# Kernel tuning notes

Measured on AMD Instinct MI355X. Metric: run time of the kernel, lower is better.

## Reference

```python
import jax, jax.numpy as jnp
import numpy as np

H = 512   # hidden_size
L = 20    # num_labels
B, S = 32, 256


def _uniform(key, shape, k):
    return jax.random.uniform(key, shape, minval=-k, maxval=k, dtype=jnp.float32)


def setup_inputs() -> dict:
    key = jax.random.key(0)
    ks = iter(jax.random.split(key, 40))
    k = 1.0 / np.sqrt(H)
    inp = {
        "inputs": jax.random.normal(next(ks), (B, S, H), dtype=jnp.float32),
        "labels": jax.random.randint(next(ks), (B, S), 0, L),
        "mask": jnp.ones((B, S), dtype=jnp.int32),
    }
    for layer, din in ((0, H), (1, 2 * H)):
        for d in ("f", "b"):
            inp[f"w_ih_l{layer}{d}"] = _uniform(next(ks), (4 * H, din), k)
            inp[f"w_hh_l{layer}{d}"] = _uniform(next(ks), (4 * H, H), k)
            inp[f"b_ih_l{layer}{d}"] = _uniform(next(ks), (4 * H,), k)
            inp[f"b_hh_l{layer}{d}"] = _uniform(next(ks), (4 * H,), k)
    kf = 1.0 / np.sqrt(2 * H)
    inp["fc_w"] = _uniform(next(ks), (L, 2 * H), kf)
    inp["fc_b"] = _uniform(next(ks), (L,), kf)
    inp["trans_m"] = jax.random.normal(next(ks), (L, L), dtype=jnp.float32) * 0.1
    inp["start_scores"] = jax.random.normal(next(ks), (L,), dtype=jnp.float32) * 0.1
    inp["end_scores"] = jax.random.normal(next(ks), (L,), dtype=jnp.float32) * 0.1
    return inp


def _lstm_dir(x, wih, whh, bih, bhh, reverse):
    # x: [S, B, Din] -> hs: [S, B, H] (outputs in original time order)
    _, b, _ = x.shape
    hh = whh.shape[1]
    xw = jnp.einsum('sbd,gd->sbg', x, wih) + bih + bhh  # precompute input projections

    def step(carry, xt):
        h, c = carry
        g = xt + h @ whh.T  # [B, 4H]
        i, f, gg, o = jnp.split(g, 4, axis=-1)  # pytorch gate order i,f,g,o
        c = jax.nn.sigmoid(f) * c + jax.nn.sigmoid(i) * jnp.tanh(gg)
        h = jax.nn.sigmoid(o) * jnp.tanh(c)
        return (h, c), h

    init = (jnp.zeros((b, hh), x.dtype), jnp.zeros((b, hh), x.dtype))
    _, hs = jax.lax.scan(step, init, xw, reverse=reverse)
    return hs


def _crf_loss(logits, tags, maskf, trans, start, end):
    # logits [S,B,L], tags [S,B], maskf [S,B] float. Returns per-sample NLL [B].
    s, b, n = logits.shape
    # --- normalizer (forward algorithm) ---
    alpha0 = logits[0] + start  # [B, n]

    def step(alpha, inp):
        emit, m = inp  # emit [B,n], m [B]
        tmp = alpha[:, :, None] + trans[None, :, :] + emit[:, None, :]  # [B, from, to]
        new = jax.nn.logsumexp(tmp, axis=1)
        alpha = jnp.where(m[:, None] > 0, new, alpha)
        return alpha, None

    alpha, _ = jax.lax.scan(step, alpha0, (logits[1:], maskf[1:]))
    norm = jax.nn.logsumexp(alpha + end, axis=1)  # [B]
    # --- gold path score ---
    emit = jnp.take_along_axis(logits, tags[:, :, None], axis=2)[:, :, 0] * maskf  # [S,B]
    trans_sc = trans[tags[:-1], tags[1:]] * maskf[1:]  # [S-1,B]
    last_idx = maskf.sum(0).astype(jnp.int32) - 1  # [B]
    last_tags = tags[last_idx, jnp.arange(b)]
    gold = emit.sum(0) + trans_sc.sum(0) + start[tags[0]] + end[last_tags]
    return norm - gold


def reference(inputs, labels, mask,
              w_ih_l0f, w_hh_l0f, b_ih_l0f, b_hh_l0f,
              w_ih_l0b, w_hh_l0b, b_ih_l0b, b_hh_l0b,
              w_ih_l1f, w_hh_l1f, b_ih_l1f, b_hh_l1f,
              w_ih_l1b, w_hh_l1b, b_ih_l1b, b_hh_l1b,
              fc_w, fc_b, trans_m, start_scores, end_scores):
    x = jnp.transpose(inputs, (1, 0, 2))  # [S,B,H]
    h0 = jnp.concatenate([
        _lstm_dir(x, w_ih_l0f, w_hh_l0f, b_ih_l0f, b_hh_l0f, False),
        _lstm_dir(x, w_ih_l0b, w_hh_l0b, b_ih_l0b, b_hh_l0b, True),
    ], axis=-1)  # [S,B,2H]
    h1 = jnp.concatenate([
        _lstm_dir(h0, w_ih_l1f, w_hh_l1f, b_ih_l1f, b_hh_l1f, False),
        _lstm_dir(h0, w_ih_l1b, w_hh_l1b, b_ih_l1b, b_hh_l1b, True),
    ], axis=-1)  # [S,B,2H]
    logits = h1 @ fc_w.T + fc_b  # [S,B,L]
    tags = labels.T  # [S,B]
    maskf = mask.T.astype(logits.dtype)
    loss = _crf_loss(logits, tags, maskf, trans_m, start_scores, end_scores)
    return loss.mean()
```

## Files before the change

### kernel.cpp

```cpp
#include <hip/hip_runtime.h>

#define Sx 256
#define Bx 32
#define Hx 512
#define Gx 2048
#define Lx 20
#define Rx 8192

typedef __attribute__((ext_vector_type(8))) short short8;
typedef __attribute__((ext_vector_type(4))) float f32x4;
typedef __attribute__((ext_vector_type(16))) float f32x16;

__device__ __forceinline__ unsigned short f2bf(float f) {
  union { float f; unsigned u; } v; v.f = f;
  unsigned u = v.u;
  return (unsigned short)((u + 0x7fffu + ((u >> 16) & 1u)) >> 16);
}
__device__ __forceinline__ float bf2f(unsigned short h) {
  union { unsigned u; float f; } v; v.u = ((unsigned)h) << 16;
  return v.f;
}
__device__ __forceinline__ float bfh(unsigned long long x, int r) {
  return bf2f((unsigned short)((x >> (16 * r)) & 0xffffull));
}

__device__ __forceinline__ float fsigm(float x) {
  return __builtin_amdgcn_rcpf(1.0f + __builtin_amdgcn_exp2f(-1.44269504f * x));
}
__device__ __forceinline__ float ftanh(float x) {
  return __builtin_fmaf(-2.0f,
      __builtin_amdgcn_rcpf(1.0f + __builtin_amdgcn_exp2f(2.88539008f * x)), 1.0f);
}
#define L2E 1.44269504088896f
#define LN2 0.69314718055995f

#define GLD16(gp, lp) __builtin_amdgcn_global_load_lds( \
    (const __attribute__((address_space(1))) void*)(gp), \
    (__attribute__((address_space(3))) void*)(lp), 16, 0, 0)


__global__ void k_pack_x(const float* __restrict__ x, unsigned short* __restrict__ xbf) {
  int tid = blockIdx.x * 256 + threadIdx.x;
  int h = tid & (Hx - 1);
  int r = tid >> 9;
  int b = r & 31;
  int t = r >> 5;
  xbf[tid] = f2bf(x[(b * Sx + t) * Hx + h]);
}

__global__ __launch_bounds__(256) void k_prep(
    const float* __restrict__ s0, const float* __restrict__ s1,
    const float* __restrict__ s2, const float* __restrict__ s3,
    const float* __restrict__ s4, const float* __restrict__ s5,
    const float* __restrict__ s6, const float* __restrict__ s7,
    unsigned short* __restrict__ d0, unsigned short* __restrict__ d1,
    unsigned short* __restrict__ d2, unsigned short* __restrict__ d3,
    unsigned short* __restrict__ d4, unsigned short* __restrict__ d5,
    unsigned short* __restrict__ d6, unsigned short* __restrict__ d7,
    const float* __restrict__ ba0, const float* __restrict__ bb0, float* __restrict__ bo0,
    const float* __restrict__ ba1, const float* __restrict__ bb1, float* __restrict__ bo1,
    const float* __restrict__ ba2, const float* __restrict__ bb2, float* __restrict__ bo2,
    const float* __restrict__ ba3, const float* __restrict__ bb3, float* __restrict__ bo3)
{
  const int blk = blockIdx.x;
  const int tid = threadIdx.x;
  if (blk < 5120) {
    const float* srcs[8] = { s0, s1, s2, s3, s4, s5, s6, s7 };
    unsigned short* dsts[8] = { d0, d1, d2, d3, d4, d5, d6, d7 };
    size_t e0 = ((size_t)blk * 256 + tid) * 8;
    int m = (int)(e0 >> 20);
    int seg; size_t base;
    if (m < 4)      { seg = m; base = (size_t)m << 20; }
    else if (m < 6) { seg = 4; base = (size_t)4 << 20; }
    else if (m < 8) { seg = 5; base = (size_t)6 << 20; }
    else if (m == 8){ seg = 6; base = (size_t)8 << 20; }
    else            { seg = 7; base = (size_t)9 << 20; }
    size_t off = e0 - base;
    f32x4 a = *(const f32x4*)(srcs[seg] + off);
    f32x4 b = *(const f32x4*)(srcs[seg] + off + 4);
    short8 o;
    o[0] = (short)f2bf(a[0]); o[1] = (short)f2bf(a[1]);
    o[2] = (short)f2bf(a[2]); o[3] = (short)f2bf(a[3]);
    o[4] = (short)f2bf(b[0]); o[5] = (short)f2bf(b[1]);
    o[6] = (short)f2bf(b[2]); o[7] = (short)f2bf(b[3]);
    *(short8*)(dsts[seg] + off) = o;
  } else {
    int j = blk - 5120;
    const float* bas[4] = { ba0, ba1, ba2, ba3 };
    const float* bbs[4] = { bb0, bb1, bb2, bb3 };
    float* bos[4] = { bo0, bo1, bo2, bo3 };
    int i0 = tid * 8;
    f32x4 x0 = *(const f32x4*)(bas[j] + i0);
    f32x4 x1 = *(const f32x4*)(bas[j] + i0 + 4);
    f32x4 y0 = *(const f32x4*)(bbs[j] + i0);
    f32x4 y1 = *(const f32x4*)(bbs[j] + i0 + 4);
    *(f32x4*)(bos[j] + i0) = x0 + y0;
    *(f32x4*)(bos[j] + i0 + 4) = x1 + y1;
  }
}

__global__ __launch_bounds__(256) void k_gemm(
    const unsigned short* __restrict__ A,
    const unsigned short* __restrict__ Bw,
    const float* __restrict__ bias,
    unsigned short* __restrict__ C,
    int M, int N, int K)
{
  const int bn = blockIdx.x, bm = blockIdx.y;
  const int tid = threadIdx.x;
  const int w = tid >> 6, lane = tid & 63;
  const int wr = w >> 1, wc = w & 1;
  const int lo = lane & 15, qd = lane >> 4;

  __shared__ unsigned short As[128 * 64];
  __shared__ unsigned short Bs[128 * 64];

  f32x4 acc[4][4] = {};

  const int cis = (lane & 7) ^ (lane >> 3);
  const int ktn = K >> 6;
  for (int kt = 0; kt < ktn; ++kt) {
    __syncthreads();
#pragma unroll
    for (int p = 0; p < 4; ++p) {
      int rowb = w * 8 + p * 32;
      int row = rowb + (lane >> 3);
      GLD16(&A[(size_t)(bm * 128 + row) * K + kt * 64 + cis * 8], &As[rowb * 64]);
      GLD16(&Bw[(size_t)(bn * 128 + row) * K + kt * 64 + cis * 8], &Bs[rowb * 64]);
    }
    __syncthreads();
#pragma unroll
    for (int kk = 0; kk < 2; ++kk) {
      short8 af[4], bfr[4];
#pragma unroll
      for (int mi = 0; mi < 4; ++mi)
        af[mi] = *(const short8*)&As[(wr * 64 + mi * 16 + lo) * 64
                                     + (((kk * 4 + qd) ^ (lo & 7)) * 8)];
#pragma unroll
      for (int ni = 0; ni < 4; ++ni)
        bfr[ni] = *(const short8*)&Bs[(wc * 64 + ni * 16 + lo) * 64
                                      + (((kk * 4 + qd) ^ (lo & 7)) * 8)];
#pragma unroll
      for (int mi = 0; mi < 4; ++mi)
#pragma unroll
        for (int ni = 0; ni < 4; ++ni)
          acc[mi][ni] = __builtin_amdgcn_mfma_f32_16x16x32_bf16(af[mi], bfr[ni], acc[mi][ni], 0, 0, 0);
    }
  }
#pragma unroll
  for (int mi = 0; mi < 4; ++mi) {
#pragma unroll
    for (int ni = 0; ni < 4; ++ni) {
      int n = bn * 128 + wc * 64 + ni * 16 + lo;
      float bv = bias[n];
      int wsb = (n >> 4) & 31, cg = n >> 9, jl = n & 15;
      size_t base = (size_t)wsb * (Rx * 64) + (size_t)cg * 16 + jl;
#pragma unroll
      for (int r = 0; r < 4; ++r) {
        int m = bm * 128 + wr * 64 + mi * 16 + qd * 4 + r;
        C[base + (size_t)m * 64] = f2bf(acc[mi][ni][r] + bv);
      }
    }
  }
}

__global__ __launch_bounds__(256, 1) void k_lstm(
    const unsigned short* __restrict__ xwF,
    const unsigned short* __restrict__ xwB,
    const unsigned short* __restrict__ whF,
    const unsigned short* __restrict__ whB,
    unsigned short* __restrict__ hT,
    unsigned int* __restrict__ flags,
    unsigned int* __restrict__ done,
    const unsigned short* __restrict__ gWf,
    const unsigned short* __restrict__ gWb,
    const float* __restrict__ gBf,
    const float* __restrict__ gBb,
    unsigned short* __restrict__ gCf,
    unsigned short* __restrict__ gCb,
    unsigned int* __restrict__ wq,
    int gw)
{
  const int wg = blockIdx.x;
  const int tid = threadIdx.x;

  __shared__ unsigned short Ws[64 * 512];
  __shared__ unsigned widx;

  if (wg >= 64) {
    asm volatile("s_setprio 0");
    if (gw) {
      const int w = tid >> 6, lane = tid & 63;
      const int wr = w >> 1, wc = w & 1;
      const int lo = lane & 15, qd = lane >> 4;
      const int cis = (lane & 7) ^ (lane >> 3);
      for (;;) {
        if (tid == 0) widx = atomicAdd(wq, 1u);
        __syncthreads();
        unsigned idx = widx;
        __syncthreads();
        if (idx >= 2048u) break;
        int r = (int)(idx >> 5), sub = (int)(idx & 31);
        int dir1 = sub >> 4, bn = sub & 15;
        int bm = (r & 1) ? (32 - ((r + 1) >> 1)) : (32 + (r >> 1));
        unsigned tF = (unsigned)(4 * bm + 4), tB = (unsigned)(256 - 4 * bm);
        if (tid < 64) {
          for (;;) {
            unsigned v = __hip_atomic_load(flags + (lane >> 5) * 1024 + (lane & 31) * 32,
                                           __ATOMIC_RELAXED, __HIP_MEMORY_SCOPE_AGENT);
            unsigned tgt = (lane < 32) ? tF : tB;
            if (__all((int)(v >= tgt))) break;
            if (__hip_atomic_load(done, __ATOMIC_RELAXED, __HIP_MEMORY_SCOPE_AGENT) >= 64u)
              break;
            float aa = 1.0f;
#pragma unroll 4
            for (int i = 0; i < 512; ++i) aa = __builtin_fmaf(aa, 1.0000001f, 1e-7f);
            asm volatile("" :: "v"(aa));
          }
        }
        __syncthreads();
        const unsigned short* Bw = dir1 ? gWb : gWf;
        const float* bias = dir1 ? gBb : gBf;
        unsigned short* Cq = dir1 ? gCb : gCf;
        f32x4 acc[4][4] = {};
        for (int kt = 0; kt < 16; ++kt) {
          __syncthreads();
#pragma unroll
          for (int p = 0; p < 4; ++p) {
            int rowb = w * 8 + p * 32;
            int row = rowb + (lane >> 3);
            int grow = bm * 128 + row;
            int t2 = grow >> 5, b2 = grow & 31;
            int k = kt * 64 + cis * 8;
            int dirx = k >> 9, kk2 = k & 511;
            GLD16(&hT[(size_t)dirx * (Sx * 16384) + (size_t)t2 * 16384
                      + (size_t)(kk2 >> 3) * 256 + b2 * 8], &Ws[rowb * 64]);
            GLD16(&Bw[(size_t)(bn * 128 + row) * 1024 + kt * 64 + cis * 8],
                  &Ws[8192 + rowb * 64]);
          }
          __syncthreads();
#pragma unroll
          for (int kk = 0; kk < 2; ++kk) {
            short8 af[4], bfr[4];
#pragma unroll
            for (int mi = 0; mi < 4; ++mi)
              af[mi] = *(const short8*)&Ws[(wr * 64 + mi * 16 + lo) * 64
                                           + (((kk * 4 + qd) ^ (lo & 7)) * 8)];
#pragma unroll
            for (int ni = 0; ni < 4; ++ni)
              bfr[ni] = *(const short8*)&Ws[8192 + (wc * 64 + ni * 16 + lo) * 64
                                            + (((kk * 4 + qd) ^ (lo & 7)) * 8)];
#pragma unroll
            for (int mi = 0; mi < 4; ++mi)
#pragma unroll
              for (int ni = 0; ni < 4; ++ni)
                acc[mi][ni] = __builtin_amdgcn_mfma_f32_16x16x32_bf16(af[mi], bfr[ni], acc[mi][ni], 0, 0, 0);
          }
        }
#pragma unroll
        for (int mi = 0; mi < 4; ++mi) {
#pragma unroll
          for (int ni = 0; ni < 4; ++ni) {
            int n = bn * 128 + wc * 64 + ni * 16 + lo;
            float bv = bias[n];
            int wsb = (n >> 4) & 31, cg = n >> 9, jl = n & 15;
            size_t base = (size_t)wsb * (Rx * 64) + (size_t)cg * 16 + jl;
#pragma unroll
            for (int r2 = 0; r2 < 4; ++r2) {
              int m2 = bm * 128 + wr * 64 + mi * 16 + qd * 4 + r2;
              Cq[base + (size_t)m2 * 64] = f2bf(acc[mi][ni][r2] + bv);
            }
          }
        }
        __syncthreads();
      }
    }
    {
      float a = 1.0f + (float)tid, bm2 = 1.0000001f, cm = 1.0e-7f;
      for (;;) {
#pragma unroll 8
        for (int i = 0; i < 512; ++i) a = __builtin_fmaf(a, bm2, cm);
        if (__hip_atomic_load(done, __ATOMIC_RELAXED, __HIP_MEMORY_SCOPE_AGENT) >= 64u) break;
      }
      if (a == 123.456789f) ((volatile float*)hT)[0] = a;
    }
    return;
  }

  asm volatile("s_setprio 3");
  const int dir = wg >> 5;
  const int vs = wg & 31;
  const int j0 = vs * 16;
  const unsigned short* xw = (dir ? xwB : xwF) + (size_t)vs * (Rx * 64);
  const unsigned short* wh = dir ? whB : whF;
  unsigned short* hTd = hT + (size_t)dir * (Sx * 16384);
  unsigned int* fl = flags + dir * 32 * 32;

  {
    const int l6 = tid & 63;
#pragma unroll
    for (int i = 0; i < 16; ++i) {
      int rr = (tid >> 6) * 16 + i;
      int g = ((rr >> 4) << 9) + j0 + (rr & 15);
      int pc = l6 ^ (rr & 7);
      *(short8*)&Ws[rr * 512 + pc * 8] = *(const short8*)&wh[(size_t)g * Hx + l6 * 8];
    }
  }
  __syncthreads();
  if (tid >= 64) return;

  const int lane = tid;
  const int bn = lane & 31;
  const int q  = lane >> 5;

  float cst[2][4] = {};

  for (int s = 0; s < Sx; ++s) {
    const int t = dir ? (Sx - 1 - s) : s;

    const unsigned short* xwt = xw + ((size_t)t * 32 + bn) * 64 + q * 4;
    unsigned long long xg[4][2];
#pragma unroll
    for (int c = 0; c < 4; ++c)
#pragma unroll
      for (int jg = 0; jg < 2; ++jg)
        xg[c][jg] = *(const unsigned long long*)(xwt + c * 16 + jg * 8);
    __asm__ __volatile__("" ::: "memory");

    f32x16 acc0, acc1;

    if (s > 0) {
      const unsigned tgt = (unsigned)s;
      const int tp = dir ? (t + 1) : (t - 1);
      const unsigned short* hb = hTd + (size_t)tp * 16384 + lane * 8;

      short8 hreg[32];
      for (;;) {
        unsigned v = __hip_atomic_load(fl + (lane & 31) * 32,
                                       __ATOMIC_RELAXED, __HIP_MEMORY_SCOPE_AGENT);
#pragma unroll
        for (int ks = 0; ks < 32; ++ks)
          hreg[ks] = *(const short8*)(hb + ks * 512);
#pragma unroll
        for (int ks = 0; ks < 32; ++ks)
          asm volatile("" :: "v"(hreg[ks]));
        if (__all((int)(v >= tgt))) break;
        __asm__ __volatile__("" ::: "memory");
      }
      __builtin_amdgcn_sched_barrier(0);

      f32x16 a0 = {}, a1 = {}, b0 = {}, b1 = {};
#pragma unroll
      for (int ks = 0; ks < 32; ks += 2) {
        int lc0 = ks * 2 + q, lc1 = (ks + 1) * 2 + q;
        int pc0 = lc0 ^ (bn & 7), pc1 = lc1 ^ (bn & 7);
        short8 af00 = *(const short8*)&Ws[bn * 512 + pc0 * 8];
        short8 af10 = *(const short8*)&Ws[(32 + bn) * 512 + pc0 * 8];
        short8 af01 = *(const short8*)&Ws[bn * 512 + pc1 * 8];
        short8 af11 = *(const short8*)&Ws[(32 + bn) * 512 + pc1 * 8];
        a0 = __builtin_amdgcn_mfma_f32_32x32x16_bf16(af00, hreg[ks],     a0, 0, 0, 0);
        a1 = __builtin_amdgcn_mfma_f32_32x32x16_bf16(af10, hreg[ks],     a1, 0, 0, 0);
        b0 = __builtin_amdgcn_mfma_f32_32x32x16_bf16(af01, hreg[ks + 1], b0, 0, 0, 0);
        b1 = __builtin_amdgcn_mfma_f32_32x32x16_bf16(af11, hreg[ks + 1], b1, 0, 0, 0);
      }
      acc0 = a0 + b0;
      acc1 = a1 + b1;
    } else {
      acc0 = (f32x16){};
      acc1 = (f32x16){};
    }

#pragma unroll
    for (int jg = 0; jg < 2; ++jg) {
      unsigned long long hv = 0;
#pragma unroll
      for (int r = 0; r < 4; ++r) {
        float iv = acc0[jg * 4 + r]     + bfh(xg[0][jg], r);
        float fv = acc0[8 + jg * 4 + r] + bfh(xg[1][jg], r);
        float gv = acc1[jg * 4 + r]     + bfh(xg[2][jg], r);
        float ov = acc1[8 + jg * 4 + r] + bfh(xg[3][jg], r);
        float ct = fsigm(fv) * cst[jg][r] + fsigm(iv) * ftanh(gv);
        cst[jg][r] = ct;
        float hvf = fsigm(ov) * ftanh(ct);
        hv |= (unsigned long long)f2bf(hvf) << (16 * r);
      }
      unsigned short* hw = hTd + (size_t)t * 16384 + ((size_t)(vs * 2 + jg) * 32 + bn) * 8 + q * 4;
      __hip_atomic_store((unsigned long long*)hw, hv,
                         __ATOMIC_RELAXED, __HIP_MEMORY_SCOPE_AGENT);
    }

    __asm__ __volatile__("s_waitcnt vmcnt(0)" ::: "memory");
    if (lane == 0)
      __hip_atomic_store(fl + vs * 32, (unsigned)(s + 1),
                         __ATOMIC_RELAXED, __HIP_MEMORY_SCOPE_AGENT);
  }

  if (lane == 0)
    __hip_atomic_fetch_add(done, 1u, __ATOMIC_RELAXED, __HIP_MEMORY_SCOPE_AGENT);
}

__global__ __launch_bounds__(256) void k_fc(
    const unsigned short* __restrict__ h1T,
    const float* __restrict__ fcw,
    const float* __restrict__ fcb,
    float* __restrict__ logits)
{
  int row = blockIdx.x;
  int t = row >> 5, b = row & 31;
  int l = threadIdx.x & 31;
  int sl = threadIdx.x >> 5;
  __shared__ float red[8][32];
  float p = 0.f;
  if (l < Lx) {
#pragma unroll 4
    for (int kt = sl * 16; kt < sl * 16 + 16; ++kt) {
      int k = kt * 8;
      int dir = k >> 9, kk = k & 511;
      const unsigned short* hp = h1T + (size_t)dir * (Sx * 16384) + (size_t)t * 16384
                                 + ((size_t)(kk >> 3) * 32 + b) * 8;
      short8 hv = *(const short8*)hp;
      const float* wr = fcw + l * 1024 + k;
      f32x4 w0 = *(const f32x4*)wr;
      f32x4 w1 = *(const f32x4*)(wr + 4);
      p += bf2f((unsigned short)hv[0]) * w0[0] + bf2f((unsigned short)hv[1]) * w0[1]
         + bf2f((unsigned short)hv[2]) * w0[2] + bf2f((unsigned short)hv[3]) * w0[3]
         + bf2f((unsigned short)hv[4]) * w1[0] + bf2f((unsigned short)hv[5]) * w1[1]
         + bf2f((unsigned short)hv[6]) * w1[2] + bf2f((unsigned short)hv[7]) * w1[3];
    }
  }
  red[sl][l] = p;
  __syncthreads();
  if (threadIdx.x < Lx) {
    float s = fcb[threadIdx.x];
#pragma unroll
    for (int i = 0; i < 8; ++i) s += red[i][threadIdx.x];
    logits[(size_t)row * Lx + threadIdx.x] = s;
  }
}

__global__ __launch_bounds__(64) void k_crf(
    const float* __restrict__ logits,
    const int* __restrict__ labels,
    const int* __restrict__ mask,
    const float* __restrict__ trans,
    const float* __restrict__ startv,
    const float* __restrict__ endv,
    float* __restrict__ out)
{
  int b = blockIdx.x;
  int tid = threadIdx.x;
  __shared__ float tr[Lx * Lx];
  __shared__ float al[2][Lx];
  __shared__ float norm_s;
  for (int i = tid; i < Lx * Lx; i += 64) tr[i] = trans[i];
  if (tid < Lx) al[0][tid] = logits[b * Lx + tid] + startv[tid];
  __syncthreads();
  int cur = 0;
  float em = (tid < Lx) ? logits[((size_t)1 * Bx + b) * Lx + tid] : 0.f;
  int m = mask[b * Sx + 1];
  for (int t = 1; t < Sx; ++t) {
    float em_next = 0.f;
    int m_next = 0;
    if (t + 1 < Sx) {
      if (tid < Lx) em_next = logits[((size_t)(t + 1) * Bx + b) * Lx + tid];
      m_next = mask[b * Sx + t + 1];
    }
    if (tid < Lx) {
      int to = tid;
      float v[Lx];
      float mx = -1e30f;
#pragma unroll
      for (int f = 0; f < Lx; ++f) { v[f] = al[cur][f] + tr[f * Lx + to]; mx = fmaxf(mx, v[f]); }
      float sum = 0.f;
#pragma unroll
      for (int f = 0; f < Lx; ++f) sum += __builtin_amdgcn_exp2f((v[f] - mx) * L2E);
      float nv = mx + LN2 * __builtin_amdgcn_logf(sum) + em;
      al[1 - cur][to] = (m > 0) ? nv : al[cur][to];
    }
    __syncthreads();
    cur ^= 1;
    em = em_next;
    m = m_next;
  }
  if (tid == 0) {
    float mx = -1e30f;
    for (int l = 0; l < Lx; ++l) mx = fmaxf(mx, al[cur][l] + endv[l]);
    float s = 0.f;
    for (int l = 0; l < Lx; ++l) s += __builtin_amdgcn_exp2f((al[cur][l] + endv[l] - mx) * L2E);
    norm_s = mx + LN2 * __builtin_amdgcn_logf(s);
  }
  __syncthreads();
  const int* lab = labels + b * Sx;
  const int* msk = mask + b * Sx;
  float part = 0.f;
  int msum = 0;
  for (int t = tid; t < Sx; t += 64) {
    int mm = msk[t];
    int tg = lab[t];
    if (mm > 0) {
      part += logits[((size_t)t * Bx + b) * Lx + tg];
      if (t >= 1) part += tr[lab[t - 1] * Lx + tg];
      msum++;
    }
  }
#pragma unroll
  for (int o = 32; o > 0; o >>= 1) {
    part += __shfl_down(part, o, 64);
    msum += __shfl_down(msum, o, 64);
  }
  if (tid == 0) {
    float gold = part + startv[lab[0]] + endv[lab[msum - 1]];
    atomicAdd(out, (norm_s - gold) * (1.0f / 32.0f));
  }
}


extern "C" void kernel_launch(void* const* d_in, const int* in_sizes, int n_in,
                              void* d_out, int out_size, void* d_ws, size_t ws_size,
                              hipStream_t stream)
{
  const float* x      = (const float*)d_in[0];
  const int* labels   = (const int*)d_in[1];
  const int* mask     = (const int*)d_in[2];
  const float* wih0f  = (const float*)d_in[3];
  const float* whh0f  = (const float*)d_in[4];
  const float* bih0f  = (const float*)d_in[5];
  const float* bhh0f  = (const float*)d_in[6];
  const float* wih0b  = (const float*)d_in[7];
  const float* whh0b  = (const float*)d_in[8];
  const float* bih0b  = (const float*)d_in[9];
  const float* bhh0b  = (const float*)d_in[10];
  const float* wih1f  = (const float*)d_in[11];
  const float* whh1f  = (const float*)d_in[12];
  const float* bih1f  = (const float*)d_in[13];
  const float* bhh1f  = (const float*)d_in[14];
  const float* wih1b  = (const float*)d_in[15];
  const float* whh1b  = (const float*)d_in[16];
  const float* bih1b  = (const float*)d_in[17];
  const float* bhh1b  = (const float*)d_in[18];
  const float* fcw    = (const float*)d_in[19];
  const float* fcb    = (const float*)d_in[20];
  const float* transm = (const float*)d_in[21];
  const float* startv = (const float*)d_in[22];
  const float* endv   = (const float*)d_in[23];

  char* p = (char*)d_ws;
  auto alloc = [&](size_t bytes) -> char* {
    char* r = p;
    p += (bytes + 255) & ~((size_t)255);
    return r;
  };

  unsigned short* x_bf    = (unsigned short*)alloc((size_t)Rx * Hx * 2);
  unsigned short* wih0f_b = (unsigned short*)alloc((size_t)Gx * Hx * 2);
  unsigned short* wih0b_b = (unsigned short*)alloc((size_t)Gx * Hx * 2);
  unsigned short* whh0f_b = (unsigned short*)alloc((size_t)Gx * Hx * 2);
  unsigned short* whh0b_b = (unsigned short*)alloc((size_t)Gx * Hx * 2);
  unsigned short* wih1f_b = (unsigned short*)alloc((size_t)Gx * 1024 * 2);
  unsigned short* wih1b_b = (unsigned short*)alloc((size_t)Gx * 1024 * 2);
  unsigned short* whh1f_b = (unsigned short*)alloc((size_t)Gx * Hx * 2);
  unsigned short* whh1b_b = (unsigned short*)alloc((size_t)Gx * Hx * 2);
  float* bias0f = (float*)alloc(Gx * 4);
  float* bias0b = (float*)alloc(Gx * 4);
  float* bias1f = (float*)alloc(Gx * 4);
  float* bias1b = (float*)alloc(Gx * 4);
  unsigned short* xw_f  = (unsigned short*)alloc((size_t)Rx * Gx * 2);
  unsigned short* xw_b  = (unsigned short*)alloc((size_t)Rx * Gx * 2);
  unsigned short* xw1_f = (unsigned short*)alloc((size_t)Rx * Gx * 2);
  unsigned short* xw1_b = (unsigned short*)alloc((size_t)Rx * Gx * 2);
  unsigned short* h0T  = (unsigned short*)alloc((size_t)2 * Sx * 16384 * 2);
  unsigned short* h1T  = (unsigned short*)alloc((size_t)2 * Sx * 16384 * 2);
  float* logits = (float*)alloc((size_t)Rx * Lx * 4);
  unsigned int* flagsA = (unsigned int*)alloc(2 * 32 * 32 * 4);
  unsigned int* flagsB = (unsigned int*)alloc(2 * 32 * 32 * 4);
  unsigned int* doneA  = (unsigned int*)alloc(256);
  unsigned int* doneB  = (unsigned int*)alloc(256);
  unsigned int* wq     = (unsigned int*)alloc(256);

  if ((size_t)(p - (char*)d_ws) > ws_size) return;

  hipMemsetAsync(flagsA, 0, 2 * 32 * 32 * 4, stream);
  hipMemsetAsync(flagsB, 0, 2 * 32 * 32 * 4, stream);
  hipMemsetAsync(doneA, 0, 256, stream);
  hipMemsetAsync(doneB, 0, 256, stream);
  hipMemsetAsync(wq, 0, 256, stream);

  k_pack_x<<<(Rx * Hx) / 256, 256, 0, stream>>>(x, x_bf);
  k_prep<<<5124, 256, 0, stream>>>(
      wih0f, wih0b, whh0f, whh0b, wih1f, wih1b, whh1f, whh1b,
      wih0f_b, wih0b_b, whh0f_b, whh0b_b, wih1f_b, wih1b_b, whh1f_b, whh1b_b,
      bih0f, bhh0f, bias0f,
      bih0b, bhh0b, bias0b,
      bih1f, bhh1f, bias1f,
      bih1b, bhh1b, bias1b);

  k_gemm<<<dim3(Gx / 128, Rx / 128), 256, 0, stream>>>(x_bf, wih0f_b, bias0f, xw_f, Rx, Gx, Hx);
  k_gemm<<<dim3(Gx / 128, Rx / 128), 256, 0, stream>>>(x_bf, wih0b_b, bias0b, xw_b, Rx, Gx, Hx);

  k_lstm<<<256, 256, 0, stream>>>(xw_f, xw_b, whh0f_b, whh0b_b, h0T, flagsA, doneA,
                                  wih1f_b, wih1b_b, bias1f, bias1b, xw1_f, xw1_b, wq, 1);

  k_lstm<<<256, 256, 0, stream>>>(xw1_f, xw1_b, whh1f_b, whh1b_b, h1T, flagsB, doneB,
                                  (const unsigned short*)nullptr, (const unsigned short*)nullptr,
                                  (const float*)nullptr, (const float*)nullptr,
                                  (unsigned short*)nullptr, (unsigned short*)nullptr,
                                  (unsigned int*)nullptr, 0);

  k_fc<<<Rx, 256, 0, stream>>>(h1T, fcw, fcb, logits);
  hipMemsetAsync(d_out, 0, 4, stream);
  k_crf<<<Bx, 64, 0, stream>>>(logits, labels, mask, transm, startv, endv, (float*)d_out);
}
```

Before: 2.429 ms.

## Overlap layer-0 input GEMM and FC projection with LSTM recurrence via worker blocks

Removes the standalone layer-0 input-projection GEMM launches and the separate FC kernel. The layer-0 GEMM tiles are now issued from the idle worker blocks of the first LSTM kernel, ordered by time from each direction's start, and signal per-tile counters that the recurrent blocks poll before consuming each timestep. The FC logits for layer 1 are computed by worker blocks in the second LSTM kernel as soon as both directions have produced a timestep. This hides GEMM and FC time behind the serial recurrence, at the cost of extra polling in the recurrent loop and possible contention for compute units.

```diff
diff --git a/kernel.cpp b/kernel.cpp
--- a/kernel.cpp
+++ b/kernel.cpp
@@ -99,71 +99,6 @@
   }
 }
 
-__global__ __launch_bounds__(256) void k_gemm(
-    const unsigned short* __restrict__ A,
-    const unsigned short* __restrict__ Bw,
-    const float* __restrict__ bias,
-    unsigned short* __restrict__ C,
-    int M, int N, int K)
-{
-  const int bn = blockIdx.x, bm = blockIdx.y;
-  const int tid = threadIdx.x;
-  const int w = tid >> 6, lane = tid & 63;
-  const int wr = w >> 1, wc = w & 1;
-  const int lo = lane & 15, qd = lane >> 4;
-
-  __shared__ unsigned short As[128 * 64];
-  __shared__ unsigned short Bs[128 * 64];
-
-  f32x4 acc[4][4] = {};
-
-  const int cis = (lane & 7) ^ (lane >> 3);
-  const int ktn = K >> 6;
-  for (int kt = 0; kt < ktn; ++kt) {
-    __syncthreads();
-#pragma unroll
-    for (int p = 0; p < 4; ++p) {
-      int rowb = w * 8 + p * 32;
-      int row = rowb + (lane >> 3);
-      GLD16(&A[(size_t)(bm * 128 + row) * K + kt * 64 + cis * 8], &As[rowb * 64]);
-      GLD16(&Bw[(size_t)(bn * 128 + row) * K + kt * 64 + cis * 8], &Bs[rowb * 64]);
-    }
-    __syncthreads();
-#pragma unroll
-    for (int kk = 0; kk < 2; ++kk) {
-      short8 af[4], bfr[4];
-#pragma unroll
-      for (int mi = 0; mi < 4; ++mi)
-        af[mi] = *(const short8*)&As[(wr * 64 + mi * 16 + lo) * 64
-                                     + (((kk * 4 + qd) ^ (lo & 7)) * 8)];
-#pragma unroll
-      for (int ni = 0; ni < 4; ++ni)
-        bfr[ni] = *(const short8*)&Bs[(wc * 64 + ni * 16 + lo) * 64
-                                      + (((kk * 4 + qd) ^ (lo & 7)) * 8)];
-#pragma unroll
-      for (int mi = 0; mi < 4; ++mi)
-#pragma unroll
-        for (int ni = 0; ni < 4; ++ni)
-          acc[mi][ni] = __builtin_amdgcn_mfma_f32_16x16x32_bf16(af[mi], bfr[ni], acc[mi][ni], 0, 0, 0);
-    }
-  }
-#pragma unroll
-  for (int mi = 0; mi < 4; ++mi) {
-#pragma unroll
-    for (int ni = 0; ni < 4; ++ni) {
-      int n = bn * 128 + wc * 64 + ni * 16 + lo;
-      float bv = bias[n];
-      int wsb = (n >> 4) & 31, cg = n >> 9, jl = n & 15;
-      size_t base = (size_t)wsb * (Rx * 64) + (size_t)cg * 16 + jl;
-#pragma unroll
-      for (int r = 0; r < 4; ++r) {
-        int m = bm * 128 + wr * 64 + mi * 16 + qd * 4 + r;
-        C[base + (size_t)m * 64] = f2bf(acc[mi][ni][r] + bv);
-      }
-    }
-  }
-}
-
 __global__ __launch_bounds__(256, 1) void k_lstm(
     const unsigned short* __restrict__ xwF,
     const unsigned short* __restrict__ xwB,
@@ -172,14 +107,19 @@
     unsigned short* __restrict__ hT,
     unsigned int* __restrict__ flags,
     unsigned int* __restrict__ done,
-    const unsigned short* __restrict__ gWf,
-    const unsigned short* __restrict__ gWb,
-    const float* __restrict__ gBf,
-    const float* __restrict__ gBb,
-    unsigned short* __restrict__ gCf,
-    unsigned short* __restrict__ gCb,
+    int mode,
+    const unsigned short* __restrict__ xA,
+    const unsigned short* __restrict__ gW0f, const unsigned short* __restrict__ gW0b,
+    const float* __restrict__ gB0f, const float* __restrict__ gB0b,
+    unsigned short* __restrict__ gC0f, unsigned short* __restrict__ gC0b,
+    const unsigned short* __restrict__ gW1f, const unsigned short* __restrict__ gW1b,
+    const float* __restrict__ gB1f, const float* __restrict__ gB1b,
+    unsigned short* __restrict__ gC1f, unsigned short* __restrict__ gC1b,
+    unsigned int* __restrict__ xq,
     unsigned int* __restrict__ wq,
-    int gw)
+    const float* __restrict__ fcw,
+    const float* __restrict__ fcb,
+    float* __restrict__ logits)
 {
   const int wg = blockIdx.x;
   const int tid = threadIdx.x;
@@ -189,7 +129,7 @@
 
   if (wg >= 64) {
     asm volatile("s_setprio 0");
-    if (gw) {
+    if (mode == 1) {
       const int w = tid >> 6, lane = tid & 63;
       const int wr = w >> 1, wc = w & 1;
       const int lo = lane & 15, qd = lane >> 4;
@@ -199,11 +139,151 @@
         __syncthreads();
         unsigned idx = widx;
         __syncthreads();
-        if (idx >= 2048u) break;
-        int r = (int)(idx >> 5), sub = (int)(idx & 31);
-        int dir1 = sub >> 4, bn = sub & 15;
-        int bm = (r & 1) ? (32 - ((r + 1) >> 1)) : (32 + (r >> 1));
-        unsigned tF = (unsigned)(4 * bm + 4), tB = (unsigned)(256 - 4 * bm);
+        if (idx >= 4096u) break;
+        if (idx < 2048u) {
+          int j = (int)(idx >> 4), bn = (int)(idx & 15);
+          int dir0 = j & 1;
+          int bm = dir0 ? (63 - (j >> 1)) : (j >> 1);
+          const unsigned short* Bw = dir0 ? gW0b : gW0f;
+          const float* bias = dir0 ? gB0b : gB0f;
+          unsigned short* Cq = dir0 ? gC0b : gC0f;
+          f32x4 acc[4][4] = {};
+          for (int kt = 0; kt < 8; ++kt) {
+            __syncthreads();
+#pragma unroll
+            for (int p = 0; p < 4; ++p) {
+              int rowb = w * 8 + p * 32;
+              int row = rowb + (lane >> 3);
+              GLD16(&xA[(size_t)(bm * 128 + row) * 512 + kt * 64 + cis * 8], &Ws[rowb * 64]);
+              GLD16(&Bw[(size_t)(bn * 128 + row) * 512 + kt * 64 + cis * 8],
+                    &Ws[8192 + rowb * 64]);
+            }
+            __syncthreads();
+#pragma unroll
+            for (int kk = 0; kk < 2; ++kk) {
+              short8 af[4], bfr[4];
+#pragma unroll
+              for (int mi = 0; mi < 4; ++mi)
+                af[mi] = *(const short8*)&Ws[(wr * 64 + mi * 16 + lo) * 64
+                                             + (((kk * 4 + qd) ^ (lo & 7)) * 8)];
+#pragma unroll
+              for (int ni = 0; ni < 4; ++ni)
+                bfr[ni] = *(const short8*)&Ws[8192 + (wc * 64 + ni * 16 + lo) * 64
+                                              + (((kk * 4 + qd) ^ (lo & 7)) * 8)];
+#pragma unroll
+              for (int mi = 0; mi < 4; ++mi)
+#pragma unroll
+                for (int ni = 0; ni < 4; ++ni)
+                  acc[mi][ni] = __builtin_amdgcn_mfma_f32_16x16x32_bf16(af[mi], bfr[ni], acc[mi][ni], 0, 0, 0);
+            }
+          }
+#pragma unroll
+          for (int mi = 0; mi < 4; ++mi) {
+#pragma unroll
+            for (int ni = 0; ni < 4; ++ni) {
+              int n = bn * 128 + wc * 64 + ni * 16 + lo;
+              float bv = bias[n];
+              int wsb = (n >> 4) & 31, cg = n >> 9, jl = n & 15;
+              size_t base = (size_t)wsb * (Rx * 64) + (size_t)cg * 16 + jl;
+#pragma unroll
+              for (int r2 = 0; r2 < 4; ++r2) {
+                int m2 = bm * 128 + wr * 64 + mi * 16 + qd * 4 + r2;
+                Cq[base + (size_t)m2 * 64] = f2bf(acc[mi][ni][r2] + bv);
+              }
+            }
+          }
+          __syncthreads();
+          if (tid == 0)
+            __hip_atomic_fetch_add(xq + dir0 * 64 + bm, 1u,
+                                   __ATOMIC_RELEASE, __HIP_MEMORY_SCOPE_AGENT);
+        } else {
+          unsigned idx2 = idx - 2048u;
+          int r = (int)(idx2 >> 5), sub = (int)(idx2 & 31);
+          int dir1 = sub >> 4, bn = sub & 15;
+          int bm = (r & 1) ? (32 - ((r + 1) >> 1)) : (32 + (r >> 1));
+          unsigned tF = (unsigned)(4 * bm + 4), tB = (unsigned)(256 - 4 * bm);
+          if (tid < 64) {
+            for (;;) {
+              unsigned v = __hip_atomic_load(flags + (lane >> 5) * 1024 + (lane & 31) * 32,
+                                             __ATOMIC_RELAXED, __HIP_MEMORY_SCOPE_AGENT);
+              unsigned tgt = (lane < 32) ? tF : tB;
+              if (__all((int)(v >= tgt))) break;
+              if (__hip_atomic_load(done, __ATOMIC_RELAXED, __HIP_MEMORY_SCOPE_AGENT) >= 64u)
+                break;
+              float aa = 1.0f;
+#pragma unroll 4
+              for (int i = 0; i < 512; ++i) aa = __builtin_fmaf(aa, 1.0000001f, 1e-7f);
+              asm volatile("" :: "v"(aa));
+            }
+          }
+          __syncthreads();
+          const unsigned short* Bw = dir1 ? gW1b : gW1f;
+          const float* bias = dir1 ? gB1b : gB1f;
+          unsigned short* Cq = dir1 ? gC1b : gC1f;
+          f32x4 acc[4][4] = {};
+          for (int kt = 0; kt < 16; ++kt) {
+            __syncthreads();
+#pragma unroll
+            for (int p = 0; p < 4; ++p) {
+              int rowb = w * 8 + p * 32;
+              int row = rowb + (lane >> 3);
+              int grow = bm * 128 + row;
+              int t2 = grow >> 5, b2 = grow & 31;
+              int k = kt * 64 + cis * 8;
+              int dirx = k >> 9, kk2 = k & 511;
+              GLD16(&hT[(size_t)dirx * (Sx * 16384) + (size_t)t2 * 16384
+                        + (size_t)(kk2 >> 3) * 256 + b2 * 8], &Ws[rowb * 64]);
+              GLD16(&Bw[(size_t)(bn * 128 + row) * 1024 + kt * 64 + cis * 8],
+                    &Ws[8192 + rowb * 64]);
+            }
+            __syncthreads();
+#pragma unroll
+            for (int kk = 0; kk < 2; ++kk) {
+              short8 af[4], bfr[4];
+#pragma unroll
+              for (int mi = 0; mi < 4; ++mi)
+                af[mi] = *(const short8*)&Ws[(wr * 64 + mi * 16 + lo) * 64
+                                             + (((kk * 4 + qd) ^ (lo & 7)) * 8)];
+#pragma unroll
+              for (int ni = 0; ni < 4; ++ni)
+                bfr[ni] = *(const short8*)&Ws[8192 + (wc * 64 + ni * 16 + lo) * 64
+                                              + (((kk * 4 + qd) ^ (lo & 7)) * 8)];
+#pragma unroll
+              for (int mi = 0; mi < 4; ++mi)
+#pragma unroll
+                for (int ni = 0; ni < 4; ++ni)
+                  acc[mi][ni] = __builtin_amdgcn_mfma_f32_16x16x32_bf16(af[mi], bfr[ni], acc[mi][ni], 0, 0, 0);
+            }
+          }
+#pragma unroll
+          for (int mi = 0; mi < 4; ++mi) {
+#pragma unroll
+            for (int ni = 0; ni < 4; ++ni) {
+              int n = bn * 128 + wc * 64 + ni * 16 + lo;
+              float bv = bias[n];
+              int wsb = (n >> 4) & 31, cg = n >> 9, jl = n & 15;
+              size_t base = (size_t)wsb * (Rx * 64) + (size_t)cg * 16 + jl;
+#pragma unroll
+              for (int r2 = 0; r2 < 4; ++r2) {
+                int m2 = bm * 128 + wr * 64 + mi * 16 + qd * 4 + r2;
+                Cq[base + (size_t)m2 * 64] = f2bf(acc[mi][ni][r2] + bv);
+              }
+            }
+          }
+        }
+        __syncthreads();
+      }
+    } else if (mode == 2) {
+      const int lane = tid & 63;
+      for (;;) {
+        if (tid == 0) widx = atomicAdd(wq, 1u);
+        __syncthreads();
+        unsigned idx = widx;
+        __syncthreads();
+        if (idx >= 256u) break;
+        int r = (int)idx;
+        int t = (r & 1) ? (127 - (r >> 1)) : (128 + (r >> 1));
+        unsigned tF = (unsigned)(t + 1), tB = (unsigned)(Sx - t);
         if (tid < 64) {
           for (;;) {
             unsigned v = __hip_atomic_load(flags + (lane >> 5) * 1024 + (lane & 31) * 32,
@@ -219,58 +299,27 @@
           }
         }
         __syncthreads();
-        const unsigned short* Bw = dir1 ? gWb : gWf;
-        const float* bias = dir1 ? gBb : gBf;
-        unsigned short* Cq = dir1 ? gCb : gCf;
-        f32x4 acc[4][4] = {};
-        for (int kt = 0; kt < 16; ++kt) {
-          __syncthreads();
-#pragma unroll
-          for (int p = 0; p < 4; ++p) {
-            int rowb = w * 8 + p * 32;
-            int row = rowb + (lane >> 3);
-            int grow = bm * 128 + row;
-            int t2 = grow >> 5, b2 = grow & 31;
-            int k = kt * 64 + cis * 8;
-            int dirx = k >> 9, kk2 = k & 511;
-            GLD16(&hT[(size_t)dirx * (Sx * 16384) + (size_t)t2 * 16384
-                      + (size_t)(kk2 >> 3) * 256 + b2 * 8], &Ws[rowb * 64]);
-            GLD16(&Bw[(size_t)(bn * 128 + row) * 1024 + kt * 64 + cis * 8],
-                  &Ws[8192 + rowb * 64]);
+#pragma unroll
+        for (int i = 0; i < 16; ++i) {
+          int cidx = i * 256 + tid;
+          int d2 = cidx >> 11, c2 = cidx & 2047;
+          *(short8*)&Ws[cidx * 8] =
+              *(const short8*)&hT[(size_t)d2 * (Sx * 16384) + (size_t)t * 16384
+                                  + (size_t)c2 * 8];
+        }
+        __syncthreads();
+        for (int o = tid; o < 640; o += 256) {
+          int b2 = o / 20, l2 = o - b2 * 20;
+          float accf = fcb[l2];
+          for (int kc = 0; kc < 128; ++kc) {
+            short8 hv = *(const short8*)&Ws[(((kc >> 6) * 2048) + (kc & 63) * 32 + b2) * 8];
+            const float* wr2 = fcw + l2 * 1024 + (kc >> 6) * 512 + (kc & 63) * 8;
+            accf += bf2f((unsigned short)hv[0]) * wr2[0] + bf2f((unsigned short)hv[1]) * wr2[1]
+                  + bf2f((unsigned short)hv[2]) * wr2[2] + bf2f((unsigned short)hv[3]) * wr2[3]
+                  + bf2f((unsigned short)hv[4]) * wr2[4] + bf2f((unsigned short)hv[5]) * wr2[5]
+                  + bf2f((unsigned short)hv[6]) * wr2[6] + bf2f((unsigned short)hv[7]) * wr2[7];
           }
-          __syncthreads();
-#pragma unroll
-          for (int kk = 0; kk < 2; ++kk) {
-            short8 af[4], bfr[4];
-#pragma unroll
-            for (int mi = 0; mi < 4; ++mi)
-              af[mi] = *(const short8*)&Ws[(wr * 64 + mi * 16 + lo) * 64
-                                           + (((kk * 4 + qd) ^ (lo & 7)) * 8)];
-#pragma unroll
-            for (int ni = 0; ni < 4; ++ni)
-              bfr[ni] = *(const short8*)&Ws[8192 + (wc * 64 + ni * 16 + lo) * 64
-                                            + (((kk * 4 + qd) ^ (lo & 7)) * 8)];
-#pragma unroll
-            for (int mi = 0; mi < 4; ++mi)
-#pragma unroll
-              for (int ni = 0; ni < 4; ++ni)
-                acc[mi][ni] = __builtin_amdgcn_mfma_f32_16x16x32_bf16(af[mi], bfr[ni], acc[mi][ni], 0, 0, 0);
-          }
-        }
-#pragma unroll
-        for (int mi = 0; mi < 4; ++mi) {
-#pragma unroll
-          for (int ni = 0; ni < 4; ++ni) {
-            int n = bn * 128 + wc * 64 + ni * 16 + lo;
-            float bv = bias[n];
-            int wsb = (n >> 4) & 31, cg = n >> 9, jl = n & 15;
-            size_t base = (size_t)wsb * (Rx * 64) + (size_t)cg * 16 + jl;
-#pragma unroll
-            for (int r2 = 0; r2 < 4; ++r2) {
-              int m2 = bm * 128 + wr * 64 + mi * 16 + qd * 4 + r2;
-              Cq[base + (size_t)m2 * 64] = f2bf(acc[mi][ni][r2] + bv);
-            }
-          }
+          logits[((size_t)t * 32 + b2) * 20 + l2] = accf;
         }
         __syncthreads();
       }
@@ -295,6 +344,7 @@
   const unsigned short* wh = dir ? whB : whF;
   unsigned short* hTd = hT + (size_t)dir * (Sx * 16384);
   unsigned int* fl = flags + dir * 32 * 32;
+  const unsigned int* xwc = xq ? (xq + dir * 64) : (const unsigned int*)0;
 
   {
     const int l6 = tid & 63;
@@ -313,6 +363,14 @@
   const int bn = lane & 31;
   const int q  = lane >> 5;
 
+  if (xwc) {
+    unsigned v;
+    do {
+      v = __hip_atomic_load(xwc + (dir ? 63 : 0),
+                            __ATOMIC_RELAXED, __HIP_MEMORY_SCOPE_AGENT);
+    } while (v < 16u);
+  }
+
   float cst[2][4] = {};
 
   for (int s = 0; s < Sx; ++s) {
@@ -336,15 +394,25 @@
 
       short8 hreg[32];
       for (;;) {
-        unsigned v = __hip_atomic_load(fl + (lane & 31) * 32,
-                                       __ATOMIC_RELAXED, __HIP_MEMORY_SCOPE_AGENT);
+        unsigned v, tgt2;
+        if (lane < 32 || !xwc) {
+          v = __hip_atomic_load(fl + (lane & 31) * 32,
+                                __ATOMIC_RELAXED, __HIP_MEMORY_SCOPE_AGENT);
+          tgt2 = tgt;
+        } else {
+          int sn = (s + 1 < Sx) ? (s + 1) : (Sx - 1);
+          int tn = dir ? (Sx - 1 - sn) : sn;
+          v = __hip_atomic_load(xwc + (tn >> 2),
+                                __ATOMIC_RELAXED, __HIP_MEMORY_SCOPE_AGENT);
+          tgt2 = 16u;
+        }
 #pragma unroll
         for (int ks = 0; ks < 32; ++ks)
           hreg[ks] = *(const short8*)(hb + ks * 512);
 #pragma unroll
         for (int ks = 0; ks < 32; ++ks)
           asm volatile("" :: "v"(hreg[ks]));
-        if (__all((int)(v >= tgt))) break;
+        if (__all((int)(v >= tgt2))) break;
         __asm__ __volatile__("" ::: "memory");
       }
       __builtin_amdgcn_sched_barrier(0);
@@ -397,45 +465,6 @@
 
   if (lane == 0)
     __hip_atomic_fetch_add(done, 1u, __ATOMIC_RELAXED, __HIP_MEMORY_SCOPE_AGENT);
-}
-
-__global__ __launch_bounds__(256) void k_fc(
-    const unsigned short* __restrict__ h1T,
-    const float* __restrict__ fcw,
-    const float* __restrict__ fcb,
-    float* __restrict__ logits)
-{
-  int row = blockIdx.x;
-  int t = row >> 5, b = row & 31;
-  int l = threadIdx.x & 31;
-  int sl = threadIdx.x >> 5;
-  __shared__ float red[8][32];
-  float p = 0.f;
-  if (l < Lx) {
-#pragma unroll 4
-    for (int kt = sl * 16; kt < sl * 16 + 16; ++kt) {
-      int k = kt * 8;
-      int dir = k >> 9, kk = k & 511;
-      const unsigned short* hp = h1T + (size_t)dir * (Sx * 16384) + (size_t)t * 16384
-                                 + ((size_t)(kk >> 3) * 32 + b) * 8;
-      short8 hv = *(const short8*)hp;
-      const float* wr = fcw + l * 1024 + k;
-      f32x4 w0 = *(const f32x4*)wr;
-      f32x4 w1 = *(const f32x4*)(wr + 4);
-      p += bf2f((unsigned short)hv[0]) * w0[0] + bf2f((unsigned short)hv[1]) * w0[1]
-         + bf2f((unsigned short)hv[2]) * w0[2] + bf2f((unsigned short)hv[3]) * w0[3]
-         + bf2f((unsigned short)hv[4]) * w1[0] + bf2f((unsigned short)hv[5]) * w1[1]
-         + bf2f((unsigned short)hv[6]) * w1[2] + bf2f((unsigned short)hv[7]) * w1[3];
-    }
-  }
-  red[sl][l] = p;
-  __syncthreads();
-  if (threadIdx.x < Lx) {
-    float s = fcb[threadIdx.x];
-#pragma unroll
-    for (int i = 0; i < 8; ++i) s += red[i][threadIdx.x];
-    logits[(size_t)row * Lx + threadIdx.x] = s;
-  }
 }
 
 __global__ __launch_bounds__(64) void k_crf(
@@ -575,7 +604,8 @@
   unsigned int* flagsB = (unsigned int*)alloc(2 * 32 * 32 * 4);
   unsigned int* doneA  = (unsigned int*)alloc(256);
   unsigned int* doneB  = (unsigned int*)alloc(256);
-  unsigned int* wq     = (unsigned int*)alloc(256);
+  unsigned int* wq     = (unsigned int*)alloc(512);
+  unsigned int* xwcnt  = (unsigned int*)alloc(2 * 64 * 4);
 
   if ((size_t)(p - (char*)d_ws) > ws_size) return;
 
@@ -583,7 +613,8 @@
   hipMemsetAsync(flagsB, 0, 2 * 32 * 32 * 4, stream);
   hipMemsetAsync(doneA, 0, 256, stream);
   hipMemsetAsync(doneB, 0, 256, stream);
-  hipMemsetAsync(wq, 0, 256, stream);
+  hipMemsetAsync(wq, 0, 512, stream);
+  hipMemsetAsync(xwcnt, 0, 2 * 64 * 4, stream);
 
   k_pack_x<<<(Rx * Hx) / 256, 256, 0, stream>>>(x, x_bf);
   k_prep<<<5124, 256, 0, stream>>>(
@@ -594,19 +625,24 @@
       bih1f, bhh1f, bias1f,
       bih1b, bhh1b, bias1b);
 
-  k_gemm<<<dim3(Gx / 128, Rx / 128), 256, 0, stream>>>(x_bf, wih0f_b, bias0f, xw_f, Rx, Gx, Hx);
-  k_gemm<<<dim3(Gx / 128, Rx / 128), 256, 0, stream>>>(x_bf, wih0b_b, bias0b, xw_b, Rx, Gx, Hx);
-
-  k_lstm<<<256, 256, 0, stream>>>(xw_f, xw_b, whh0f_b, whh0b_b, h0T, flagsA, doneA,
-                                  wih1f_b, wih1b_b, bias1f, bias1b, xw1_f, xw1_b, wq, 1);
-
-  k_lstm<<<256, 256, 0, stream>>>(xw1_f, xw1_b, whh1f_b, whh1b_b, h1T, flagsB, doneB,
+  k_lstm<<<256, 256, 0, stream>>>(xw_f, xw_b, whh0f_b, whh0b_b, h0T, flagsA, doneA, 1,
+                                  x_bf, wih0f_b, wih0b_b, bias0f, bias0b, xw_f, xw_b,
+                                  wih1f_b, wih1b_b, bias1f, bias1b, xw1_f, xw1_b,
+                                  xwcnt, wq,
+                                  (const float*)nullptr, (const float*)nullptr,
+                                  (float*)nullptr);
+
+  k_lstm<<<256, 256, 0, stream>>>(xw1_f, xw1_b, whh1f_b, whh1b_b, h1T, flagsB, doneB, 2,
+                                  (const unsigned short*)nullptr,
                                   (const unsigned short*)nullptr, (const unsigned short*)nullptr,
                                   (const float*)nullptr, (const float*)nullptr,
                                   (unsigned short*)nullptr, (unsigned short*)nullptr,
-                                  (unsigned int*)nullptr, 0);
-
-  k_fc<<<Rx, 256, 0, stream>>>(h1T, fcw, fcb, logits);
+                                  (const unsigned short*)nullptr, (const unsigned short*)nullptr,
+                                  (const float*)nullptr, (const float*)nullptr,
+                                  (unsigned short*)nullptr, (unsigned short*)nullptr,
+                                  (unsigned int*)nullptr, wq + 64,
+                                  fcw, fcb, logits);
+
   hipMemsetAsync(d_out, 0, 4, stream);
   k_crf<<<Bx, 64, 0, stream>>>(logits, labels, mask, transm, startv, endv, (float*)d_out);
 }
```

After: 2.469 ms. No clear change (+1.7%).
